# Kernel optimization log

Hardware: AMD Instinct MI355X
Metric: run time of the kernel (lower is better)

The kernel has to match this reference:

```python
import math
import jax, jax.numpy as jnp
import numpy as np

SCALE = 64.0
MARGIN = 0.5
T = 0.2
COS_M = math.cos(MARGIN)
SIN_M = math.sin(MARGIN)
TH = math.cos(math.pi - MARGIN)
MM = math.sin(math.pi - MARGIN) * MARGIN
EPS = 1e-07

B, D, C = 512, 512, 100000


def setup_inputs() -> dict:
    key = jax.random.key(0)
    k1, k2, k3 = jax.random.split(key, 3)
    embedding = jax.random.normal(k1, (B, D), dtype=jnp.float32)
    # xavier_uniform for (num_classes, embed_size)
    limit = math.sqrt(6.0 / (C + D))
    weight = jax.random.uniform(k2, (C, D), dtype=jnp.float32, minval=-limit, maxval=limit)
    ground_truth = jax.random.randint(k3, (B,), 0, C, dtype=jnp.int64)
    return {"embedding": embedding, "weight": weight, "ground_truth": ground_truth}


def reference(embedding, weight, ground_truth):
    gt = ground_truth.astype(jnp.int32)
    e = embedding / jnp.linalg.norm(embedding, axis=1, keepdims=True)
    w = weight / jnp.linalg.norm(weight, axis=1, keepdims=True)
    # (B, C) cosine similarities
    cos_theta = jnp.clip(jnp.einsum('bd,cd->bc', e, w), -1.0 + EPS, 1.0 - EPS)
    pos = jnp.take_along_axis(cos_theta, gt[:, None], axis=1)  # (B, 1)
    sin_theta = jnp.sqrt(jnp.clip(1.0 - pos * pos, EPS, 1.0 - EPS))
    phi = pos * COS_M - sin_theta * SIN_M
    phi = jnp.where(pos > TH, phi, pos - MM)  # easy_margin=False branch
    # hard-example reweighting: fixed=False -> (t+1)*cos + t where cos > phi
    mask = cos_theta > phi  # phi broadcasts (B,1) -> (B,C)
    cos_theta = jnp.where(mask, (T + 1.0) * cos_theta + T, cos_theta)
    # scatter phi into the ground-truth column
    output = cos_theta.at[jnp.arange(B), gt].set(phi[:, 0])
    output = output * SCALE
    # mean cross-entropy
    logp = jax.nn.log_softmax(output, axis=1)
    loss = -jnp.mean(jnp.take_along_axis(logp, gt[:, None], axis=1))
    return loss
```

## Files before the change

### kernel.cpp

```cpp
#include <hip/hip_runtime.h>
#include <hip/hip_bf16.h>
#include <stdint.h>

typedef unsigned short u16;
typedef __attribute__((ext_vector_type(8))) short short8;
typedef __attribute__((ext_vector_type(4))) float floatx4;

#define B_   512
#define D_   512
#define C_   100000

#define SCALE_  64.0f
#define COSM_   0.8775825618903728f
#define SINM_   0.479425538604203f
#define TH_     (-0.8775825618903728f)
#define MM_     0.2397127693021015f
#define EPS_    1e-7f
#define SHIFT_  89.6f

#define BM 256
#define BN 64

__device__ inline float wave_reduce_sum(float v) {
    v += __shfl_xor(v, 1);
    v += __shfl_xor(v, 2);
    v += __shfl_xor(v, 4);
    v += __shfl_xor(v, 8);
    v += __shfl_xor(v, 16);
    v += __shfl_xor(v, 32);
    return v;
}

__device__ inline u16 f2bf(float x) {
    union { float f; uint32_t u; } v; v.f = x;
    uint32_t r = v.u + 0x7fffu + ((v.u >> 16) & 1u);
    return (u16)(r >> 16);
}

__device__ inline uint32_t cvt2_rn(float a, float b) {
    union { __hip_bfloat162 h; uint32_t u; } v;
    v.h = __float22bfloat162_rn(make_float2(a, b));
    return v.u;
}

__global__ __launch_bounds__(256) void norm_e_phi_kernel(
    const float* __restrict__ emb, const float* __restrict__ w_raw,
    const int* __restrict__ gt, u16* __restrict__ e_bf16,
    float* __restrict__ phi, float* __restrict__ rowsum) {
    if (threadIdx.x < 4) rowsum[blockIdx.x * 4 + threadIdx.x] = 0.0f;
    int wv = threadIdx.x >> 6;
    int lane = threadIdx.x & 63;
    int b = blockIdx.x * 4 + wv;
    const float4* rp = (const float4*)(emb + (long)b * D_);
    float4 f0 = rp[lane], f1 = rp[lane + 64];
    float sq = f0.x*f0.x + f0.y*f0.y + f0.z*f0.z + f0.w*f0.w
             + f1.x*f1.x + f1.y*f1.y + f1.z*f1.z + f1.w*f1.w;
    sq = wave_reduce_sum(sq);
    float rn = 1.0f / sqrtf(sq);
    f0.x *= rn; f0.y *= rn; f0.z *= rn; f0.w *= rn;
    f1.x *= rn; f1.y *= rn; f1.z *= rn; f1.w *= rn;
    uint2 p0, p1;
    p0.x = (uint32_t)f2bf(f0.x) | ((uint32_t)f2bf(f0.y) << 16);
    p0.y = (uint32_t)f2bf(f0.z) | ((uint32_t)f2bf(f0.w) << 16);
    p1.x = (uint32_t)f2bf(f1.x) | ((uint32_t)f2bf(f1.y) << 16);
    p1.y = (uint32_t)f2bf(f1.z) | ((uint32_t)f2bf(f1.w) << 16);
    uint2* ob = (uint2*)(e_bf16 + (long)b * D_);
    ob[lane] = p0;
    ob[lane + 64] = p1;

    int g = gt[b];
    const float4* wp = (const float4*)(w_raw + (long)g * D_);
    float4 w0 = wp[lane], w1 = wp[lane + 64];
    float dt = f0.x*w0.x + f0.y*w0.y + f0.z*w0.z + f0.w*w0.w
             + f1.x*w1.x + f1.y*w1.y + f1.z*w1.z + f1.w*w1.w;
    float wsq = w0.x*w0.x + w0.y*w0.y + w0.z*w0.z + w0.w*w0.w
              + w1.x*w1.x + w1.y*w1.y + w1.z*w1.z + w1.w*w1.w;
    dt = wave_reduce_sum(dt);
    wsq = wave_reduce_sum(wsq);
    if (lane == 0) {
        float pos = dt / sqrtf(wsq);
        pos = fminf(fmaxf(pos, -1.0f + EPS_), 1.0f - EPS_);
        float s2 = 1.0f - pos * pos;
        s2 = fminf(fmaxf(s2, EPS_), 1.0f - EPS_);
        float sin_t = sqrtf(s2);
        float ph = pos * COSM_ - sin_t * SINM_;
        ph = (pos > TH_) ? ph : (pos - MM_);
        phi[b] = ph;
    }
}

__global__ __launch_bounds__(256, 2) void gemm_arcface_fused(
    const u16* __restrict__ a_g,
    const float* __restrict__ w_g,
    const float* __restrict__ phi, const int* __restrict__ gt,
    float* __restrict__ rowsum) {
    __shared__ float phi_s[BM];
    __shared__ int gt_s[BM];

    int tid = threadIdx.x;
    int c0 = (blockIdx.x >> 1) * BN;
    int m0 = (blockIdx.x & 1) * BM;

    phi_s[tid] = phi[m0 + tid];
    gt_s[tid] = gt[m0 + tid];
    __syncthreads();

    int wv = tid >> 6, lane = tid & 63;
    int low4 = lane & 15, quad = lane >> 4;

    const u16* a_base = a_g + (long)(m0 + wv * 64 + low4) * D_ + quad * 8;
    const float4* bp[4];
#pragma unroll
    for (int ni = 0; ni < 4; ni++) {
        int row = min(c0 + ni * 16 + low4, C_ - 1);
        bp[ni] = (const float4*)(w_g + (long)row * D_ + quad * 8);
    }

    floatx4 acc[4][4] = {};
    float sq[4] = {0.0f, 0.0f, 0.0f, 0.0f};

#pragma unroll
    for (int kt = 0; kt < 16; kt++) {
        short8 af[4];
#pragma unroll
        for (int mi = 0; mi < 4; mi++)
            af[mi] = *(const short8*)(a_base + (long)mi * 16 * D_ + kt * 32);
        short8 bfr[4];
#pragma unroll
        for (int ni = 0; ni < 4; ni++) {
            float4 lo = bp[ni][kt * 8];
            float4 hi = bp[ni][kt * 8 + 1];
            sq[ni] += lo.x*lo.x + lo.y*lo.y + lo.z*lo.z + lo.w*lo.w
                    + hi.x*hi.x + hi.y*hi.y + hi.z*hi.z + hi.w*hi.w;
            union { short8 s; uint32_t u[4]; } bb;
            bb.u[0] = cvt2_rn(lo.x, lo.y);
            bb.u[1] = cvt2_rn(lo.z, lo.w);
            bb.u[2] = cvt2_rn(hi.x, hi.y);
            bb.u[3] = cvt2_rn(hi.z, hi.w);
            bfr[ni] = bb.s;
        }
#pragma unroll
        for (int mi = 0; mi < 4; mi++)
#pragma unroll
            for (int ni = 0; ni < 4; ni++)
                acc[mi][ni] = __builtin_amdgcn_mfma_f32_16x16x32_bf16(
                    af[mi], bfr[ni], acc[mi][ni], 0, 0, 0);
    }

    float rnorm[4];
#pragma unroll
    for (int ni = 0; ni < 4; ni++) {
        float s = sq[ni];
        s += __shfl_xor(s, 16);
        s += __shfl_xor(s, 32);
        rnorm[ni] = 1.0f / sqrtf(s);
    }

#pragma unroll
    for (int mi = 0; mi < 4; mi++) {
#pragma unroll
        for (int r = 0; r < 4; r++) {
            int rl = wv * 64 + mi * 16 + quad * 4 + r;
            float ph = phi_s[rl];
            int g = gt_s[rl];
            float s = 0.0f;
#pragma unroll
            for (int ni = 0; ni < 4; ni++) {
                int cl = ni * 16 + low4;
                int c = c0 + cl;
                float v = acc[mi][ni][r] * rnorm[ni];
                v = fminf(fmaxf(v, -1.0f + EPS_), 1.0f - EPS_);
                float logit = (v > ph) ? (1.2f * v + 0.2f) : v;
                logit *= SCALE_;
                if (c == g) logit = SCALE_ * ph;
                s += (c < C_) ? __expf(logit - SHIFT_) : 0.0f;
            }
            s += __shfl_xor(s, 1);
            s += __shfl_xor(s, 2);
            s += __shfl_xor(s, 4);
            s += __shfl_xor(s, 8);
            if (low4 == 0) atomicAdd(&rowsum[m0 + rl], s);
        }
    }
}

__global__ __launch_bounds__(256) void loss_kernel(
    const float* __restrict__ rowsum, const float* __restrict__ phi,
    float* __restrict__ out) {
    __shared__ float red[4];
    int tid = threadIdx.x;
    float s = 0.0f;
    for (int b = tid; b < B_; b += 256)
        s += logf(rowsum[b]) + SHIFT_ - SCALE_ * phi[b];
    s = wave_reduce_sum(s);
    int wv = tid >> 6, lane = tid & 63;
    if (lane == 0) red[wv] = s;
    __syncthreads();
    if (tid == 0) out[0] = (red[0] + red[1] + red[2] + red[3]) * (1.0f / B_);
}

extern "C" void kernel_launch(void* const* d_in, const int* in_sizes, int n_in,
                              void* d_out, int out_size, void* d_ws, size_t ws_size,
                              hipStream_t stream) {
    const float* emb = (const float*)d_in[0];
    const float* wgt = (const float*)d_in[1];
    const int* gt = (const int*)d_in[2];
    float* out = (float*)d_out;

    char* ws = (char*)d_ws;
    u16* e_bf16 = (u16*)(ws);
    float* phi = (float*)(ws + 524288);
    float* rowsum = (float*)(ws + 526336);

    norm_e_phi_kernel<<<B_ / 4, 256, 0, stream>>>(emb, wgt, gt, e_bf16, phi, rowsum);
    int nc = (C_ + BN - 1) / BN;
    gemm_arcface_fused<<<nc * 2, 256, 0, stream>>>(e_bf16, wgt, phi, gt, rowsum);
    loss_kernel<<<1, 256, 0, stream>>>(rowsum, phi, out);
}
```

Baseline: 524.0 us.

## Stage weight tiles through double-buffered LDS via direct global-to-LDS loads

Instead of every wave reading the fp32 weight rows from global memory into registers, the block now cooperatively loads each 64x32 weight tile with global_load_lds into a swizzled, double-buffered LDS array and prefetches the next k-slice while the current one is computed. This removes the four-fold redundant global reads across waves and overlaps the loads with compute. The MFMA issue is also interleaved per weight fragment. The cost is a __syncthreads per k-step and 16KB of extra LDS, which may reduce occupancy or add stalls.

```diff
diff --git a/kernel.cpp b/kernel.cpp
--- a/kernel.cpp
+++ b/kernel.cpp
@@ -20,6 +20,11 @@
 
 #define BM 256
 #define BN 64
+#define BK 32
+
+#define GLDS16(gsrc, ldst) __builtin_amdgcn_global_load_lds(                 \
+    (const __attribute__((address_space(1))) uint32_t*)(gsrc),               \
+    (__attribute__((address_space(3))) uint32_t*)(ldst), 16, 0, 0)
 
 __device__ inline float wave_reduce_sum(float v) {
     v += __shfl_xor(v, 1);
@@ -94,6 +99,7 @@
     const float* __restrict__ w_g,
     const float* __restrict__ phi, const int* __restrict__ gt,
     float* __restrict__ rowsum) {
+    __shared__ __align__(16) float btile[2][BN * BK];
     __shared__ float phi_s[BM];
     __shared__ int gt_s[BM];
 
@@ -103,33 +109,49 @@
 
     phi_s[tid] = phi[m0 + tid];
     gt_s[tid] = gt[m0 + tid];
-    __syncthreads();
+
+    int r0 = tid >> 3;
+    int s0 = (tid & 7) ^ (r0 & 7);
+    int r1 = (tid + 256) >> 3;
+    int s1 = (tid & 7) ^ (r1 & 7);
+    const float* wsrc0 = w_g + (long)min(c0 + r0, C_ - 1) * D_ + s0 * 4;
+    const float* wsrc1 = w_g + (long)min(c0 + r1, C_ - 1) * D_ + s1 * 4;
 
     int wv = tid >> 6, lane = tid & 63;
     int low4 = lane & 15, quad = lane >> 4;
-
     const u16* a_base = a_g + (long)(m0 + wv * 64 + low4) * D_ + quad * 8;
-    const float4* bp[4];
+
+    int boff[4][2];
 #pragma unroll
     for (int ni = 0; ni < 4; ni++) {
-        int row = min(c0 + ni * 16 + low4, C_ - 1);
-        bp[ni] = (const float4*)(w_g + (long)row * D_ + quad * 8);
-    }
+        int row = ni * 16 + low4;
+        boff[ni][0] = row * BK + (((quad * 2)     ^ (row & 7)) * 4);
+        boff[ni][1] = row * BK + (((quad * 2 + 1) ^ (row & 7)) * 4);
+    }
+
+    GLDS16(wsrc0, &btile[0][0] + tid * 4);
+    GLDS16(wsrc1, &btile[0][0] + (tid + 256) * 4);
+    __syncthreads();
 
     floatx4 acc[4][4] = {};
     float sq[4] = {0.0f, 0.0f, 0.0f, 0.0f};
 
 #pragma unroll
     for (int kt = 0; kt < 16; kt++) {
+        const float* bbuf = &btile[kt & 1][0];
+        if (kt < 15) {
+            float* d0 = &btile[(kt + 1) & 1][0] + tid * 4;
+            GLDS16(wsrc0 + (kt + 1) * BK, d0);
+            GLDS16(wsrc1 + (kt + 1) * BK, d0 + 1024);
+        }
         short8 af[4];
 #pragma unroll
         for (int mi = 0; mi < 4; mi++)
-            af[mi] = *(const short8*)(a_base + (long)mi * 16 * D_ + kt * 32);
-        short8 bfr[4];
+            af[mi] = *(const short8*)(a_base + (long)mi * 16 * D_ + kt * BK);
 #pragma unroll
         for (int ni = 0; ni < 4; ni++) {
-            float4 lo = bp[ni][kt * 8];
-            float4 hi = bp[ni][kt * 8 + 1];
+            float4 lo = *(const float4*)(bbuf + boff[ni][0]);
+            float4 hi = *(const float4*)(bbuf + boff[ni][1]);
             sq[ni] += lo.x*lo.x + lo.y*lo.y + lo.z*lo.z + lo.w*lo.w
                     + hi.x*hi.x + hi.y*hi.y + hi.z*hi.z + hi.w*hi.w;
             union { short8 s; uint32_t u[4]; } bb;
@@ -137,14 +159,12 @@
             bb.u[1] = cvt2_rn(lo.z, lo.w);
             bb.u[2] = cvt2_rn(hi.x, hi.y);
             bb.u[3] = cvt2_rn(hi.z, hi.w);
-            bfr[ni] = bb.s;
+#pragma unroll
+            for (int mi = 0; mi < 4; mi++)
+                acc[mi][ni] = __builtin_amdgcn_mfma_f32_16x16x32_bf16(
+                    af[mi], bb.s, acc[mi][ni], 0, 0, 0);
         }
-#pragma unroll
-        for (int mi = 0; mi < 4; mi++)
-#pragma unroll
-            for (int ni = 0; ni < 4; ni++)
-                acc[mi][ni] = __builtin_amdgcn_mfma_f32_16x16x32_bf16(
-                    af[mi], bfr[ni], acc[mi][ni], 0, 0, 0);
+        __syncthreads();
     }
 
     float rnorm[4];
```

Measured after the change: 816.9 us. 55.9% more time.
